# Kernel optimization log

Measured on AMD Instinct MI355X. Metric: run time of the kernel, lower is better.

## Reference

```python
import jax, jax.numpy as jnp
import numpy as np

N_NODES = 100000
N_EDGES = 3200000
F_IN = 256
HID = 64
N_CLS = 16


def setup_inputs() -> dict:
    key = jax.random.key(0)
    ks = jax.random.split(key, 12)
    x = jax.random.normal(ks[0], (N_NODES, F_IN), dtype=jnp.float32)
    edge_index = jax.random.randint(ks[1], (2, N_EDGES), 0, N_NODES, dtype=jnp.int32)
    w_mul = jax.random.normal(ks[2], (N_EDGES, 1), dtype=jnp.float32)
    s1 = 1.0 / np.sqrt(F_IN)
    s2 = 1.0 / np.sqrt(HID)
    # layer 1 params
    lin1_w = jax.random.uniform(ks[3], (HID, F_IN), minval=-s1, maxval=s1, dtype=jnp.float32)
    lin1_b = jax.random.uniform(ks[4], (HID,), minval=-s1, maxval=s1, dtype=jnp.float32)
    mlp1_w0 = jax.random.uniform(ks[5], (HID, 1), minval=-1.0, maxval=1.0, dtype=jnp.float32)
    mlp1_w1 = jax.random.uniform(ks[6], (HID, HID), minval=-s2, maxval=s2, dtype=jnp.float32)
    mlp1_b1 = jax.random.uniform(ks[7], (HID,), minval=-s2, maxval=s2, dtype=jnp.float32)
    # layer 2 params
    lin2_w = jax.random.uniform(ks[8], (N_CLS, HID), minval=-s2, maxval=s2, dtype=jnp.float32)
    lin2_b = jax.random.uniform(ks[9], (N_CLS,), minval=-s2, maxval=s2, dtype=jnp.float32)
    mlp2_w0 = jax.random.uniform(ks[10], (HID, 1), minval=-1.0, maxval=1.0, dtype=jnp.float32)
    mlp2_w1 = jax.random.uniform(ks[11], (N_CLS, HID), minval=-s2, maxval=s2, dtype=jnp.float32)
    mlp2_b1 = jnp.zeros((N_CLS,), dtype=jnp.float32)
    return dict(x=x, edge_index=edge_index, w_mul=w_mul,
                lin1_w=lin1_w, lin1_b=lin1_b, mlp1_w0=mlp1_w0, mlp1_w1=mlp1_w1, mlp1_b1=mlp1_b1,
                lin2_w=lin2_w, lin2_b=lin2_b, mlp2_w0=mlp2_w0, mlp2_w1=mlp2_w1, mlp2_b1=mlp2_b1)


def curv_layer(x, src, dst, w_mul, lin_w, lin_b, m_w0, m_w1, m_b1, n_nodes):
    # dense projection: [N, out]
    h = x @ lin_w.T + lin_b
    # per-edge weight MLP: Linear(1,HID,no bias) -> LeakyReLU(0.2) -> Linear(HID,out,bias)
    ew = jax.nn.leaky_relu(w_mul @ m_w0.T, negative_slope=0.2) @ m_w1.T + m_b1  # [E, out]
    # segment softmax keyed by source node (PyG softmax(out_weight, edge_index[0]))
    emax = jax.ops.segment_max(ew, src, num_segments=n_nodes)  # [N, out]
    e = jnp.exp(ew - emax[src])
    esum = jax.ops.segment_sum(e, src, num_segments=n_nodes)
    alpha = e / (esum[src] + 1e-16)  # [E, out]
    # message = alpha * x_j (x_j = h[src]); scatter-add at destination
    msg = alpha * h[src]
    return jax.ops.segment_sum(msg, dst, num_segments=n_nodes)  # [N, out]


def reference(x, edge_index, w_mul,
              lin1_w, lin1_b, mlp1_w0, mlp1_w1, mlp1_b1,
              lin2_w, lin2_b, mlp2_w0, mlp2_w1, mlp2_b1):
    src, dst = edge_index[0], edge_index[1]
    n = x.shape[0]
    # eval mode: dropout(p=0.8) is identity
    h = curv_layer(x, src, dst, w_mul, lin1_w, lin1_b, mlp1_w0, mlp1_w1, mlp1_b1, n)
    h = jax.nn.elu(h)
    h = curv_layer(h, src, dst, w_mul, lin2_w, lin2_b, mlp2_w0, mlp2_w1, mlp2_b1, n)
    return jax.nn.log_softmax(h, axis=1)
```

## Files before the change

### kernel.cpp

```cpp
#include <hip/hip_runtime.h>
#include <math.h>

#define FIN 256
#define HID 64
#define NCLS 16
#define BSH 8
#define BWD (1 << BSH)
#define NBKMAX 512
#define CAP 9216
#define CHUNK_S 8192
#define CHUNK_D 4096

typedef __attribute__((ext_vector_type(8))) short bf16x8;
typedef __attribute__((ext_vector_type(4))) float f32x4;

__global__ __launch_bounds__(512) void init_kernel(int* gcur_s, int* gcur_d) {
    int tid = threadIdx.x;
    gcur_s[tid] = tid * CAP;
    gcur_d[tid] = tid * CAP;
}

__global__ __launch_bounds__(512) void stage_kernel(const int* __restrict__ ei,
                                                    const float* __restrict__ w,
                                                    int* gcur_s, int* gcur_d,
                                                    unsigned int* st_s, uint2* st_d,
                                                    int E, int nchunk_s) {
    __shared__ int lh[NBKMAX];
    __shared__ int lofs[NBKMAX];
    __shared__ int lcur[NBKMAX];
    __shared__ int gbase[NBKMAX];
    __shared__ int wsum[8];
    __shared__ uint2 buf2[CHUNK_D];
    unsigned int* buf1 = (unsigned int*)buf2;
    int tid = threadIdx.x;
    int wv = tid >> 6, lane = tid & 63;
    int side = (blockIdx.x >= nchunk_s) ? 1 : 0;
    lh[tid] = 0;
    __syncthreads();
    if (!side) {
        int base = blockIdx.x * CHUNK_S;
        #pragma unroll
        for (int j = 0; j < CHUNK_S / 512; j++) {
            int e = base + tid + j * 512;
            if (e < E) atomicAdd(&lh[((unsigned)ei[e]) >> BSH], 1);
        }
    } else {
        int base = (blockIdx.x - nchunk_s) * CHUNK_D;
        #pragma unroll
        for (int j = 0; j < CHUNK_D / 512; j++) {
            int e = base + tid + j * 512;
            if (e < E) atomicAdd(&lh[((unsigned)ei[E + e]) >> BSH], 1);
        }
    }
    __syncthreads();
    int v = lh[tid];
    int inc = v;
    #pragma unroll
    for (int off = 1; off < 64; off <<= 1) {
        int p = __shfl_up(inc, off);
        if (lane >= off) inc += p;
    }
    if (lane == 63) wsum[wv] = inc;
    __syncthreads();
    int pre = 0;
    #pragma unroll
    for (int j = 0; j < 8; j++) pre += (j < wv) ? wsum[j] : 0;
    int ex = pre + inc - v;
    lofs[tid] = ex;
    lcur[tid] = ex;
    __syncthreads();
    if (!side) {
        int base = blockIdx.x * CHUNK_S;
        #pragma unroll
        for (int j = 0; j < CHUNK_S / 512; j++) {
            int e = base + tid + j * 512;
            if (e < E) {
                int s = ei[e];
                unsigned int rec = (__float_as_uint(w[e]) & 0xFFFFFF00u) | (unsigned int)(s & 0xFF);
                int p = atomicAdd(&lcur[((unsigned)s) >> BSH], 1);
                buf1[p] = rec;
            }
        }
    } else {
        int base = (blockIdx.x - nchunk_s) * CHUNK_D;
        #pragma unroll
        for (int j = 0; j < CHUNK_D / 512; j++) {
            int e = base + tid + j * 512;
            if (e < E) {
                int d = ei[E + e];
                int s = ei[e];
                unsigned int rec = (__float_as_uint(w[e]) & 0xFFFFFF00u) | (unsigned int)(d & 0xFF);
                int p = atomicAdd(&lcur[((unsigned)d) >> BSH], 1);
                buf2[p] = make_uint2((unsigned int)s, rec);
            }
        }
    }
    __syncthreads();
    {
        int c = lh[tid];
        if (c) gbase[tid] = atomicAdd(side ? &gcur_d[tid] : &gcur_s[tid], c);
    }
    __syncthreads();
    int sub = lane >> 4, ln = lane & 15;
    if (!side) {
        for (int b0 = wv * 64; b0 < wv * 64 + 64; b0 += 4) {
            int b = b0 + sub;
            int c = lh[b];
            int ls = lofs[b], gs = gbase[b];
            for (int i = ln; i < c; i += 16) st_s[gs + i] = buf1[ls + i];
        }
    } else {
        for (int b0 = wv * 64; b0 < wv * 64 + 64; b0 += 4) {
            int b = b0 + sub;
            int c = lh[b];
            int ls = lofs[b], gs = gbase[b];
            for (int i = ln; i < c; i += 16) st_d[gs + i] = buf2[ls + i];
        }
    }
}

__global__ __launch_bounds__(512) void bucket_scan_kernel(const int* gcur_s, const int* gcur_d,
                                                          int* bbase_s, int* bbase_d,
                                                          int* offs_s, int* offs_d,
                                                          int N, int nbk, int E) {
    int side = blockIdx.x;
    const int* gc = side ? gcur_d : gcur_s;
    int* bb = side ? bbase_d : bbase_s;
    __shared__ int tmp[512];
    int tid = threadIdx.x;
    int v = (tid < nbk) ? (gc[tid] - tid * CAP) : 0;
    tmp[tid] = v;
    __syncthreads();
    for (int off = 1; off < 512; off <<= 1) {
        int add = (tid >= off) ? tmp[tid - off] : 0;
        __syncthreads();
        tmp[tid] += add;
        __syncthreads();
    }
    if (tid < nbk) bb[tid] = tmp[tid] - v;
    if (tid == 0) {
        bb[nbk] = E;
        (side ? offs_d : offs_s)[N] = E;
    }
}

__global__ __launch_bounds__(256) void bucket_build_s_kernel(const int* __restrict__ bbase,
                                                             const unsigned int* __restrict__ st,
                                                             int* offs, int* mid, float* t_s, int N) {
    int b = blockIdx.x;
    int r0 = bbase[b];
    int cnt = bbase[b + 1] - r0;
    if (cnt > CAP) cnt = CAP;
    size_t sb = (size_t)b * CAP;
    int n0 = b << BSH;
    int nn = min(BWD, N - n0);
    __shared__ int lh[2 * BWD];
    __shared__ int lscan[BWD];
    __shared__ int lcur[2 * BWD];
    __shared__ float buf[CAP];
    int tid = threadIdx.x;
    lh[tid] = 0;
    lh[tid + BWD] = 0;
    __syncthreads();
    for (int i = tid; i < cnt; i += 256) {
        unsigned int rec = st[sb + i];
        atomicAdd(&lh[((rec & 0xFFu) << 1) | (rec >> 31)], 1);
    }
    __syncthreads();
    int c0 = lh[2 * tid], c1 = lh[2 * tid + 1];
    int v = c0 + c1;
    lscan[tid] = v;
    __syncthreads();
    for (int off = 1; off < 256; off <<= 1) {
        int add = (tid >= off) ? lscan[tid - off] : 0;
        __syncthreads();
        lscan[tid] += add;
        __syncthreads();
    }
    int ex = lscan[tid] - v;
    if (tid < nn) {
        offs[n0 + tid] = r0 + ex;
        mid[n0 + tid] = r0 + ex + c0;
    }
    lcur[2 * tid] = ex;
    lcur[2 * tid + 1] = ex + c0;
    __syncthreads();
    for (int i = tid; i < cnt; i += 256) {
        unsigned int rec = st[sb + i];
        int p = atomicAdd(&lcur[((rec & 0xFFu) << 1) | (rec >> 31)], 1);
        buf[p] = __uint_as_float(rec & 0xFFFFFF00u);
    }
    __syncthreads();
    for (int i = tid; i < cnt; i += 256) t_s[r0 + i] = buf[i];
}

__global__ __launch_bounds__(256) void bucket_build_d_kernel(const int* __restrict__ bbase,
                                                             const uint2* __restrict__ st,
                                                             int* offs, int2* ed, int N) {
    int b = blockIdx.x;
    int r0 = bbase[b];
    int cnt = bbase[b + 1] - r0;
    if (cnt > CAP) cnt = CAP;
    size_t sb = (size_t)b * CAP;
    int n0 = b << BSH;
    int nn = min(BWD, N - n0);
    __shared__ int lh[BWD];
    __shared__ int lofs[BWD];
    __shared__ int2 buf[CAP];
    int tid = threadIdx.x;
    lh[tid] = 0;
    __syncthreads();
    for (int i = tid; i < cnt; i += 256) atomicAdd(&lh[st[sb + i].y & 0xFFu], 1);
    __syncthreads();
    int v = lh[tid];
    lofs[tid] = v;
    __syncthreads();
    for (int off = 1; off < 256; off <<= 1) {
        int add = (tid >= off) ? lofs[tid - off] : 0;
        __syncthreads();
        lofs[tid] += add;
        __syncthreads();
    }
    int ex = lofs[tid] - v;
    if (tid < nn) offs[n0 + tid] = r0 + ex;
    lofs[tid] = ex;
    __syncthreads();
    for (int i = tid; i < cnt; i += 256) {
        uint2 rec = st[sb + i];
        int p = atomicAdd(&lofs[rec.y & 0xFFu], 1);
        buf[p] = make_int2((int)rec.x, (int)(rec.y & 0xFFFFFF00u));
    }
    __syncthreads();
    for (int i = tid; i < cnt; i += 256) ed[r0 + i] = buf[i];
}

#define LOG2E 1.44269504088896340736f
__global__ void prep_kernel(const float* __restrict__ w0a, const float* __restrict__ w1a,
                            const float* __restrict__ w0b, const float* __restrict__ w1b,
                            float* Ap1, float* An1, float* Ap2, float* An2) {
    int tid = threadIdx.x;
    if (tid < 64) {
        float ap = 0.f, an = 0.f;
        for (int j = 0; j < 64; j++) {
            float w0 = w0a[j];
            float w1 = w1a[tid * 64 + j];
            ap += w0 * ((w0 >= 0.f) ? 1.f : 0.2f) * w1;
            an += w0 * ((w0 <= 0.f) ? 1.f : 0.2f) * w1;
        }
        Ap1[tid] = ap * LOG2E; An1[tid] = an * LOG2E;
    } else if (tid < 80) {
        int k = tid - 64;
        float ap = 0.f, an = 0.f;
        for (int j = 0; j < 64; j++) {
            float w0 = w0b[j];
            float w1 = w1b[k * 64 + j];
            ap += w0 * ((w0 >= 0.f) ? 1.f : 0.2f) * w1;
            an += w0 * ((w0 <= 0.f) ? 1.f : 0.2f) * w1;
        }
        Ap2[k] = ap * LOG2E; An2[k] = an * LOG2E;
    }
}

__device__ __forceinline__ float seg_expsum(const float* __restrict__ t, int i0, int i1, float a) {
    float sum = 0.f;
    int i = i0;
    for (; i + 3 < i1; i += 4) {
        float t0 = t[i], t1 = t[i + 1], t2 = t[i + 2], t3 = t[i + 3];
        sum += __builtin_amdgcn_exp2f(t0 * a);
        sum += __builtin_amdgcn_exp2f(t1 * a);
        sum += __builtin_amdgcn_exp2f(t2 * a);
        sum += __builtin_amdgcn_exp2f(t3 * a);
    }
    for (; i < i1; i++) sum += __builtin_amdgcn_exp2f(t[i] * a);
    return sum;
}

__global__ __launch_bounds__(256) void esum1_kernel(const int* __restrict__ offs,
                                                    const int* __restrict__ mid,
                                                    const float* __restrict__ t_s,
                                                    const float* __restrict__ Ap,
                                                    const float* __restrict__ An,
                                                    float* __restrict__ inv, int N) {
    int node = blockIdx.x * 4 + (threadIdx.x >> 6);
    int k = threadIdx.x & 63;
    if (node >= N) return;
    int s0 = offs[node], m = mid[node], s1 = offs[node + 1];
    float sum = seg_expsum(t_s, s0, m, Ap[k]) + seg_expsum(t_s, m, s1, An[k]);
    inv[(size_t)node * 64 + k] = (s1 > s0) ? 1.f / (sum + 1e-16f) : 0.f;
}

__global__ __launch_bounds__(256) void esum2_kernel(const int* __restrict__ offs,
                                                    const int* __restrict__ mid,
                                                    const float* __restrict__ t_s,
                                                    const float* __restrict__ Ap,
                                                    const float* __restrict__ An,
                                                    float* __restrict__ inv, int N) {
    int node = blockIdx.x * 16 + (threadIdx.x >> 4);
    int k = threadIdx.x & 15;
    if (node >= N) return;
    int s0 = offs[node], m = mid[node], s1 = offs[node + 1];
    float sum = seg_expsum(t_s, s0, m, Ap[k]) + seg_expsum(t_s, m, s1, An[k]);
    inv[(size_t)node * 16 + k] = (s1 > s0) ? 1.f / (sum + 1e-16f) : 0.f;
}

__device__ __forceinline__ unsigned int bf16rn(float f) {
    unsigned int u = __float_as_uint(f);
    return (u + 0x7fffu + ((u >> 16) & 1u)) >> 16;
}

__device__ __forceinline__ void cvt8_split(const float4 a, const float4 b, bf16x8& h, bf16x8& l) {
    float f[8] = {a.x, a.y, a.z, a.w, b.x, b.y, b.z, b.w};
    #pragma unroll
    for (int j = 0; j < 8; j++) {
        unsigned int uh = bf16rn(f[j]);
        float hf = __uint_as_float(uh << 16);
        float r = f[j] - hf;
        unsigned int ul = bf16rn(r);
        h[j] = (short)uh;
        l[j] = (short)ul;
    }
}

#define KCH 64
__global__ __launch_bounds__(256, 4) void gemm1_kernel(const float* __restrict__ x,
                                                       const float* __restrict__ W,
                                                       const float* __restrict__ b,
                                                       const float* __restrict__ inv,
                                                       uint2* __restrict__ g1, int N) {
    __shared__ unsigned short xh[64 * KCH];
    __shared__ unsigned short xl[64 * KCH];
    __shared__ unsigned short wh[64 * KCH];
    __shared__ unsigned short wl[64 * KCH];
    int tid = threadIdx.x;
    int block_row = blockIdx.x * 64;
    float4 pf[4][2];
    auto load_chunk = [&](int kbase) {
        #pragma unroll
        for (int i = 0; i < 4; i++) {
            int t = tid + i * 256;
            if (t < 512) {
                int r = t >> 3, g = t & 7;
                int gr = block_row + r;
                if (gr < N) {
                    const float* p = &x[(size_t)gr * FIN + kbase + g * 8];
                    pf[i][0] = *(const float4*)p;
                    pf[i][1] = *(const float4*)(p + 4);
                } else {
                    pf[i][0] = make_float4(0.f, 0.f, 0.f, 0.f);
                    pf[i][1] = make_float4(0.f, 0.f, 0.f, 0.f);
                }
            } else {
                int r = (t - 512) >> 3, g = t & 7;
                const float* p = &W[r * FIN + kbase + g * 8];
                pf[i][0] = *(const float4*)p;
                pf[i][1] = *(const float4*)(p + 4);
            }
        }
    };
    auto write_chunk = [&]() {
        #pragma unroll
        for (int i = 0; i < 4; i++) {
            int t = tid + i * 256;
            int r = (t & 511) >> 3, g = t & 7;
            int gs = g ^ (r & 7);
            bf16x8 h, l;
            cvt8_split(pf[i][0], pf[i][1], h, l);
            if (t < 512) {
                *(bf16x8*)&xh[r * KCH + gs * 8] = h;
                *(bf16x8*)&xl[r * KCH + gs * 8] = l;
            } else {
                *(bf16x8*)&wh[r * KCH + gs * 8] = h;
                *(bf16x8*)&wl[r * KCH + gs * 8] = l;
            }
        }
    };

    int wv = tid >> 6, l = tid & 63;
    int lrow = l & 15, kg = l >> 4;
    f32x4 acc[4];
    #pragma unroll
    for (int c = 0; c < 4; c++) acc[c] = (f32x4){0.f, 0.f, 0.f, 0.f};

    const unsigned short* xrow_h = &xh[(wv * 16 + lrow) * KCH];
    const unsigned short* xrow_l = &xl[(wv * 16 + lrow) * KCH];

    load_chunk(0);
    for (int kc = 0; kc < FIN / KCH; kc++) {
        write_chunk();
        __syncthreads();
        if (kc + 1 < FIN / KCH) load_chunk((kc + 1) * KCH);
        #pragma unroll
        for (int s = 0; s < 2; s++) {
            int gB = ((s * 4 + kg) ^ (lrow & 7)) * 8;
            bf16x8 bh = *(const bf16x8*)&xrow_h[gB];
            bf16x8 bl = *(const bf16x8*)&xrow_l[gB];
            #pragma unroll
            for (int c = 0; c < 4; c++) {
                int wro = (c * 16 + lrow) * KCH + gB;
                bf16x8 ah = *(const bf16x8*)&wh[wro];
                bf16x8 al = *(const bf16x8*)&wl[wro];
                acc[c] = __builtin_amdgcn_mfma_f32_16x16x32_bf16(ah, bh, acc[c], 0, 0, 0);
                acc[c] = __builtin_amdgcn_mfma_f32_16x16x32_bf16(ah, bl, acc[c], 0, 0, 0);
                acc[c] = __builtin_amdgcn_mfma_f32_16x16x32_bf16(al, bh, acc[c], 0, 0, 0);
            }
        }
        __syncthreads();
    }
    int node = block_row + wv * 16 + lrow;
    if (node < N) {
        #pragma unroll
        for (int c = 0; c < 4; c++) {
            int colb = c * 16 + kg * 4;
            float4 bv = *(const float4*)&b[colb];
            float4 iv = *(const float4*)&inv[(size_t)node * 64 + colb];
            float o0 = (acc[c].x + bv.x) * iv.x;
            float o1 = (acc[c].y + bv.y) * iv.y;
            float o2 = (acc[c].z + bv.z) * iv.z;
            float o3 = (acc[c].w + bv.w) * iv.w;
            uint2 p;
            p.x = bf16rn(o0) | (bf16rn(o1) << 16);
            p.y = bf16rn(o2) | (bf16rn(o3) << 16);
            g1[(size_t)node * 16 + (colb >> 2)] = p;
        }
    }
}

#define GP 68
__global__ __launch_bounds__(256) void gemm2_kernel(const float* __restrict__ x2,
                                                    const float* __restrict__ W2,
                                                    const float* __restrict__ b2,
                                                    const float* __restrict__ inv,
                                                    float* __restrict__ g2, int N) {
    __shared__ float ws[16][GP];
    __shared__ float xs[16][GP];
    __shared__ float bs[16];
    int tid = threadIdx.x;
    {
        int c = tid >> 4, j4 = tid & 15;
        float4 v = ((const float4*)W2)[tid];
        ws[c][j4 * 4 + 0] = v.x; ws[c][j4 * 4 + 1] = v.y;
        ws[c][j4 * 4 + 2] = v.z; ws[c][j4 * 4 + 3] = v.w;
    }
    if (tid < 16) bs[tid] = b2[tid];
    int node0 = blockIdx.x * 16;
    {
        int r = tid >> 4, c4 = tid & 15;
        int gn = node0 + r;
        float4 v = (gn < N) ? *(const float4*)&x2[(size_t)gn * 64 + c4 * 4]
                            : make_float4(0.f, 0.f, 0.f, 0.f);
        xs[r][c4 * 4 + 0] = v.x; xs[r][c4 * 4 + 1] = v.y;
        xs[r][c4 * 4 + 2] = v.z; xs[r][c4 * 4 + 3] = v.w;
    }
    __syncthreads();
    int node_l = tid >> 4, col = tid & 15;
    int gn = node0 + node_l;
    if (gn >= N) return;
    float acc = bs[col];
    #pragma unroll
    for (int j4 = 0; j4 < 16; j4++) {
        float4 xv = *(const float4*)&xs[node_l][j4 * 4];
        float4 wv = *(const float4*)&ws[col][j4 * 4];
        acc += xv.x * wv.x + xv.y * wv.y + xv.z * wv.z + xv.w * wv.w;
    }
    g2[(size_t)gn * NCLS + col] = acc * inv[(size_t)gn * NCLS + col];
}

__global__ __launch_bounds__(256) void agg1_kernel(const int* __restrict__ offs,
                                                   const int2* __restrict__ ed,
                                                   const float* __restrict__ Ap,
                                                   const float* __restrict__ An,
                                                   const uint4* __restrict__ g,
                                                   float* __restrict__ x2, int N) {
    int node = blockIdx.x * 32 + (threadIdx.x >> 3);
    int l = threadIdx.x & 7;
    if (node >= N) return;
    int d0 = offs[node], d1 = offs[node + 1];
    float4 ap0 = ((const float4*)Ap)[l * 2], ap1 = ((const float4*)Ap)[l * 2 + 1];
    float4 an0 = ((const float4*)An)[l * 2], an1 = ((const float4*)An)[l * 2 + 1];
    float4 acc0 = make_float4(0.f, 0.f, 0.f, 0.f);
    float4 acc1 = make_float4(0.f, 0.f, 0.f, 0.f);
    int i = d0;
    int end4 = d0 + ((d1 - d0) & ~3);
    for (; i < end4; i += 4) {
        int2 e[4];
        #pragma unroll
        for (int j = 0; j < 4; j++) e[j] = ed[i + j];
        uint4 gv[4];
        #pragma unroll
        for (int j = 0; j < 4; j++)
            gv[j] = g[((size_t)e[j].x << 3) + l];
        #pragma unroll
        for (int j = 0; j < 4; j++) {
            float t = __int_as_float(e[j].y);
            float4 a0 = (t >= 0.f) ? ap0 : an0;
            float4 a1 = (t >= 0.f) ? ap1 : an1;
            acc0.x += __builtin_amdgcn_exp2f(t * a0.x) * __uint_as_float(gv[j].x << 16);
            acc0.y += __builtin_amdgcn_exp2f(t * a0.y) * __uint_as_float(gv[j].x & 0xffff0000u);
            acc0.z += __builtin_amdgcn_exp2f(t * a0.z) * __uint_as_float(gv[j].y << 16);
            acc0.w += __builtin_amdgcn_exp2f(t * a0.w) * __uint_as_float(gv[j].y & 0xffff0000u);
            acc1.x += __builtin_amdgcn_exp2f(t * a1.x) * __uint_as_float(gv[j].z << 16);
            acc1.y += __builtin_amdgcn_exp2f(t * a1.y) * __uint_as_float(gv[j].z & 0xffff0000u);
            acc1.z += __builtin_amdgcn_exp2f(t * a1.z) * __uint_as_float(gv[j].w << 16);
            acc1.w += __builtin_amdgcn_exp2f(t * a1.w) * __uint_as_float(gv[j].w & 0xffff0000u);
        }
    }
    for (; i < d1; i++) {
        int2 e = ed[i];
        float t = __int_as_float(e.y);
        float4 a0 = (t >= 0.f) ? ap0 : an0;
        float4 a1 = (t >= 0.f) ? ap1 : an1;
        uint4 gv = g[((size_t)e.x << 3) + l];
        acc0.x += __builtin_amdgcn_exp2f(t * a0.x) * __uint_as_float(gv.x << 16);
        acc0.y += __builtin_amdgcn_exp2f(t * a0.y) * __uint_as_float(gv.x & 0xffff0000u);
        acc0.z += __builtin_amdgcn_exp2f(t * a0.z) * __uint_as_float(gv.y << 16);
        acc0.w += __builtin_amdgcn_exp2f(t * a0.w) * __uint_as_float(gv.y & 0xffff0000u);
        acc1.x += __builtin_amdgcn_exp2f(t * a1.x) * __uint_as_float(gv.z << 16);
        acc1.y += __builtin_amdgcn_exp2f(t * a1.y) * __uint_as_float(gv.z & 0xffff0000u);
        acc1.z += __builtin_amdgcn_exp2f(t * a1.z) * __uint_as_float(gv.w << 16);
        acc1.w += __builtin_amdgcn_exp2f(t * a1.w) * __uint_as_float(gv.w & 0xffff0000u);
    }
    float4 o0, o1;
    o0.x = (acc0.x > 0.f) ? acc0.x : (__expf(acc0.x) - 1.f);
    o0.y = (acc0.y > 0.f) ? acc0.y : (__expf(acc0.y) - 1.f);
    o0.z = (acc0.z > 0.f) ? acc0.z : (__expf(acc0.z) - 1.f);
    o0.w = (acc0.w > 0.f) ? acc0.w : (__expf(acc0.w) - 1.f);
    o1.x = (acc1.x > 0.f) ? acc1.x : (__expf(acc1.x) - 1.f);
    o1.y = (acc1.y > 0.f) ? acc1.y : (__expf(acc1.y) - 1.f);
    o1.z = (acc1.z > 0.f) ? acc1.z : (__expf(acc1.z) - 1.f);
    o1.w = (acc1.w > 0.f) ? acc1.w : (__expf(acc1.w) - 1.f);
    float* dst = x2 + ((size_t)node << 6) + l * 8;
    *(float4*)(dst) = o0;
    *(float4*)(dst + 4) = o1;
}

__global__ __launch_bounds__(256) void agg2_kernel(const int* __restrict__ offs,
                                                   const int2* __restrict__ ed,
                                                   const float* __restrict__ Ap,
                                                   const float* __restrict__ An,
                                                   const float* __restrict__ g,
                                                   float* __restrict__ out, int N) {
    int node = blockIdx.x * 64 + (threadIdx.x >> 2);
    int l = threadIdx.x & 3;
    if (node >= N) return;
    int d0 = offs[node], d1 = offs[node + 1];
    float4 ap = ((const float4*)Ap)[l];
    float4 an = ((const float4*)An)[l];
    float4 acc = make_float4(0.f, 0.f, 0.f, 0.f);
    int i = d0;
    int end8 = d0 + ((d1 - d0) & ~7);
    for (; i < end8; i += 8) {
        int2 e[8];
        #pragma unroll
        for (int j = 0; j < 8; j++) e[j] = ed[i + j];
        float4 gv[8];
        #pragma unroll
        for (int j = 0; j < 8; j++)
            gv[j] = *(const float4*)(g + ((size_t)e[j].x << 4) + l * 4);
        #pragma unroll
        for (int j = 0; j < 8; j++) {
            float t = __int_as_float(e[j].y);
            float4 a = (t >= 0.f) ? ap : an;
            acc.x += __builtin_amdgcn_exp2f(t * a.x) * gv[j].x;
            acc.y += __builtin_amdgcn_exp2f(t * a.y) * gv[j].y;
            acc.z += __builtin_amdgcn_exp2f(t * a.z) * gv[j].z;
            acc.w += __builtin_amdgcn_exp2f(t * a.w) * gv[j].w;
        }
    }
    for (; i < d1; i++) {
        int2 e = ed[i];
        float t = __int_as_float(e.y);
        float4 a = (t >= 0.f) ? ap : an;
        float4 gv = *(const float4*)(g + ((size_t)e.x << 4) + l * 4);
        acc.x += __builtin_amdgcn_exp2f(t * a.x) * gv.x;
        acc.y += __builtin_amdgcn_exp2f(t * a.y) * gv.y;
        acc.z += __builtin_amdgcn_exp2f(t * a.z) * gv.z;
        acc.w += __builtin_amdgcn_exp2f(t * a.w) * gv.w;
    }
    float m = fmaxf(fmaxf(acc.x, acc.y), fmaxf(acc.z, acc.w));
    m = fmaxf(m, __shfl_xor(m, 1, 4));
    m = fmaxf(m, __shfl_xor(m, 2, 4));
    float s = __expf(acc.x - m) + __expf(acc.y - m) + __expf(acc.z - m) + __expf(acc.w - m);
    s += __shfl_xor(s, 1, 4);
    s += __shfl_xor(s, 2, 4);
    float lse = m + __logf(s);
    float4 o = make_float4(acc.x - lse, acc.y - lse, acc.z - lse, acc.w - lse);
    *(float4*)(out + ((size_t)node << 4) + l * 4) = o;
}

extern "C" void kernel_launch(void* const* d_in, const int* in_sizes, int n_in,
                              void* d_out, int out_size, void* d_ws, size_t ws_size,
                              hipStream_t stream) {
    const float* x      = (const float*)d_in[0];
    const int*   ei     = (const int*)d_in[1];
    const float* wmul   = (const float*)d_in[2];
    const float* lin1_w = (const float*)d_in[3];
    const float* lin1_b = (const float*)d_in[4];
    const float* m1w0   = (const float*)d_in[5];
    const float* m1w1   = (const float*)d_in[6];
    const float* lin2_w = (const float*)d_in[8];
    const float* lin2_b = (const float*)d_in[9];
    const float* m2w0   = (const float*)d_in[10];
    const float* m2w1   = (const float*)d_in[11];

    int N = in_sizes[0] / FIN;
    int E = in_sizes[1] / 2;
    int nbk = (N + BWD - 1) >> BSH;
    int nchunk_s = (E + CHUNK_S - 1) / CHUNK_S;
    int nchunk_d = (E + CHUNK_D - 1) / CHUNK_D;

    char* ws = (char*)d_ws;
    auto alloc = [&](size_t bytes) {
        char* p = ws;
        ws += (bytes + 255) & ~(size_t)255;
        return p;
    };
    int*   gcur_s  = (int*)alloc(NBKMAX * 4);
    int*   gcur_d  = (int*)alloc(NBKMAX * 4);
    int*   bbase_s = (int*)alloc((NBKMAX + 1) * 4);
    int*   bbase_d = (int*)alloc((NBKMAX + 1) * 4);
    float* Ap1     = (float*)alloc(64 * 4);
    float* An1     = (float*)alloc(64 * 4);
    float* Ap2     = (float*)alloc(16 * 4);
    float* An2     = (float*)alloc(16 * 4);
    int*   offs_s  = (int*)alloc((size_t)(N + 1) * 4);
    int*   offs_d  = (int*)alloc((size_t)(N + 1) * 4);
    int*   mid_s   = (int*)alloc((size_t)N * 4);
    float* t_s     = (float*)alloc((size_t)E * 4);
    int2*  ed      = (int2*)alloc((size_t)E * 8);
    char*  reg = ws;
    unsigned int* st_s = (unsigned int*)(reg);
    uint2*        st_d = (uint2*)(reg + (((size_t)nbk * CAP * 4 + 255) & ~(size_t)255));
    float* inv1 = (float*)(reg);
    float* x2   = (float*)(reg);
    char*  regB = reg + (((size_t)N * 64 * 4 + 255) & ~(size_t)255);
    uint2* g1   = (uint2*)(regB);
    float* inv2 = (float*)(regB + ((size_t)N * 16 * 8));
    float* g2   = (float*)(regB + ((size_t)N * 16 * 8) + ((size_t)N * 16 * 4));

    init_kernel<<<1, 512, 0, stream>>>(gcur_s, gcur_d);
    prep_kernel<<<1, 128, 0, stream>>>(m1w0, m1w1, m2w0, m2w1, Ap1, An1, Ap2, An2);
    stage_kernel<<<nchunk_s + nchunk_d, 512, 0, stream>>>(ei, wmul, gcur_s, gcur_d,
                                                          st_s, st_d, E, nchunk_s);
    bucket_scan_kernel<<<2, 512, 0, stream>>>(gcur_s, gcur_d, bbase_s, bbase_d,
                                              offs_s, offs_d, N, nbk, E);
    bucket_build_s_kernel<<<nbk, 256, 0, stream>>>(bbase_s, st_s, offs_s, mid_s, t_s, N);
    bucket_build_d_kernel<<<nbk, 256, 0, stream>>>(bbase_d, st_d, offs_d, ed, N);
    esum1_kernel<<<(N + 3) / 4, 256, 0, stream>>>(offs_s, mid_s, t_s, Ap1, An1, inv1, N);
    gemm1_kernel<<<(N + 63) / 64, 256, 0, stream>>>(x, lin1_w, lin1_b, inv1, g1, N);
    agg1_kernel<<<(N + 31) / 32, 256, 0, stream>>>(offs_d, ed, Ap1, An1, (const uint4*)g1, x2, N);
    esum2_kernel<<<(N + 15) / 16, 256, 0, stream>>>(offs_s, mid_s, t_s, Ap2, An2, inv2, N);
    gemm2_kernel<<<(N + 15) / 16, 256, 0, stream>>>(x2, lin2_w, lin2_b, inv2, g2, N);
    agg2_kernel<<<(N + 63) / 64, 256, 0, stream>>>(offs_d, ed, Ap2, An2, g2, (float*)d_out, N);
}
```

Baseline: 487.9 us.

## Merge bucket builds and esum passes; fuse agg1 with layer-2 GEMM

Combines the source and destination bucket-build kernels into one 512-thread launch that uses a wave-shuffle scan in place of the shared-memory Hillis-Steele scan. It also merges both esum passes into one launch and fuses agg1 with gemm2, so the layer-1 output x2 stays in shared memory and never makes a round trip through global memory. This cuts launch count, global traffic for x2, and barrier-heavy scans. The trade-offs are more shared memory per block and a larger combined bucket-build buffer (int2), which may lower occupancy.

```diff
diff --git a/kernel.cpp b/kernel.cpp
--- a/kernel.cpp
+++ b/kernel.cpp
@@ -144,94 +144,86 @@
     }
 }
 
-__global__ __launch_bounds__(256) void bucket_build_s_kernel(const int* __restrict__ bbase,
-                                                             const unsigned int* __restrict__ st,
-                                                             int* offs, int* mid, float* t_s, int N) {
-    int b = blockIdx.x;
+__global__ __launch_bounds__(512) void bucket_build_kernel(const int* __restrict__ bbase_s,
+                                                           const int* __restrict__ bbase_d,
+                                                           const unsigned int* __restrict__ st_s,
+                                                           const uint2* __restrict__ st_d,
+                                                           int* offs_s, int* mid_s, int* offs_d,
+                                                           float* t_s, int2* ed, int N, int nbk) {
+    __shared__ int lh[2 * BWD];
+    __shared__ int lcur[2 * BWD];
+    __shared__ int wsum[4];
+    __shared__ int2 buf[CAP];
+    int tid = threadIdx.x;
+    int lane = tid & 63, wv = tid >> 6;
+    int sside = (blockIdx.x < nbk);
+    int b = sside ? blockIdx.x : (blockIdx.x - nbk);
+    const int* bbase = sside ? bbase_s : bbase_d;
     int r0 = bbase[b];
     int cnt = bbase[b + 1] - r0;
     if (cnt > CAP) cnt = CAP;
     size_t sb = (size_t)b * CAP;
     int n0 = b << BSH;
     int nn = min(BWD, N - n0);
-    __shared__ int lh[2 * BWD];
-    __shared__ int lscan[BWD];
-    __shared__ int lcur[2 * BWD];
-    __shared__ float buf[CAP];
-    int tid = threadIdx.x;
     lh[tid] = 0;
-    lh[tid + BWD] = 0;
-    __syncthreads();
-    for (int i = tid; i < cnt; i += 256) {
-        unsigned int rec = st[sb + i];
-        atomicAdd(&lh[((rec & 0xFFu) << 1) | (rec >> 31)], 1);
-    }
-    __syncthreads();
-    int c0 = lh[2 * tid], c1 = lh[2 * tid + 1];
-    int v = c0 + c1;
-    lscan[tid] = v;
-    __syncthreads();
-    for (int off = 1; off < 256; off <<= 1) {
-        int add = (tid >= off) ? lscan[tid - off] : 0;
+    __syncthreads();
+    if (sside) {
+        for (int i = tid; i < cnt; i += 512) {
+            unsigned int rec = st_s[sb + i];
+            atomicAdd(&lh[((rec & 0xFFu) << 1) | (rec >> 31)], 1);
+        }
+    } else {
+        for (int i = tid; i < cnt; i += 512) {
+            atomicAdd(&lh[st_d[sb + i].y & 0xFFu], 1);
+        }
+    }
+    __syncthreads();
+    int c0 = 0, v = 0, inc = 0;
+    if (tid < 256) {
+        if (sside) { c0 = lh[2 * tid]; v = c0 + lh[2 * tid + 1]; }
+        else { v = lh[tid]; }
+        inc = v;
+        #pragma unroll
+        for (int off = 1; off < 64; off <<= 1) {
+            int p = __shfl_up(inc, off);
+            if (lane >= off) inc += p;
+        }
+        if (lane == 63) wsum[wv] = inc;
+    }
+    __syncthreads();
+    if (tid < 256) {
+        int pre = 0;
+        #pragma unroll
+        for (int j = 0; j < 4; j++) pre += (j < wv) ? wsum[j] : 0;
+        int ex = pre + inc - v;
+        if (sside) {
+            if (tid < nn) { offs_s[n0 + tid] = r0 + ex; mid_s[n0 + tid] = r0 + ex + c0; }
+            lcur[2 * tid] = ex;
+            lcur[2 * tid + 1] = ex + c0;
+        } else {
+            if (tid < nn) offs_d[n0 + tid] = r0 + ex;
+            lcur[tid] = ex;
+        }
+    }
+    __syncthreads();
+    if (sside) {
+        float* buff = (float*)buf;
+        for (int i = tid; i < cnt; i += 512) {
+            unsigned int rec = st_s[sb + i];
+            int p = atomicAdd(&lcur[((rec & 0xFFu) << 1) | (rec >> 31)], 1);
+            buff[p] = __uint_as_float(rec & 0xFFFFFF00u);
+        }
         __syncthreads();
-        lscan[tid] += add;
+        for (int i = tid; i < cnt; i += 512) t_s[r0 + i] = buff[i];
+    } else {
+        for (int i = tid; i < cnt; i += 512) {
+            uint2 rec = st_d[sb + i];
+            int p = atomicAdd(&lcur[rec.y & 0xFFu], 1);
+            buf[p] = make_int2((int)rec.x, (int)(rec.y & 0xFFFFFF00u));
+        }
         __syncthreads();
-    }
-    int ex = lscan[tid] - v;
-    if (tid < nn) {
-        offs[n0 + tid] = r0 + ex;
-        mid[n0 + tid] = r0 + ex + c0;
-    }
-    lcur[2 * tid] = ex;
-    lcur[2 * tid + 1] = ex + c0;
-    __syncthreads();
-    for (int i = tid; i < cnt; i += 256) {
-        unsigned int rec = st[sb + i];
-        int p = atomicAdd(&lcur[((rec & 0xFFu) << 1) | (rec >> 31)], 1);
-        buf[p] = __uint_as_float(rec & 0xFFFFFF00u);
-    }
-    __syncthreads();
-    for (int i = tid; i < cnt; i += 256) t_s[r0 + i] = buf[i];
-}
-
-__global__ __launch_bounds__(256) void bucket_build_d_kernel(const int* __restrict__ bbase,
-                                                             const uint2* __restrict__ st,
-                                                             int* offs, int2* ed, int N) {
-    int b = blockIdx.x;
-    int r0 = bbase[b];
-    int cnt = bbase[b + 1] - r0;
-    if (cnt > CAP) cnt = CAP;
-    size_t sb = (size_t)b * CAP;
-    int n0 = b << BSH;
-    int nn = min(BWD, N - n0);
-    __shared__ int lh[BWD];
-    __shared__ int lofs[BWD];
-    __shared__ int2 buf[CAP];
-    int tid = threadIdx.x;
-    lh[tid] = 0;
-    __syncthreads();
-    for (int i = tid; i < cnt; i += 256) atomicAdd(&lh[st[sb + i].y & 0xFFu], 1);
-    __syncthreads();
-    int v = lh[tid];
-    lofs[tid] = v;
-    __syncthreads();
-    for (int off = 1; off < 256; off <<= 1) {
-        int add = (tid >= off) ? lofs[tid - off] : 0;
-        __syncthreads();
-        lofs[tid] += add;
-        __syncthreads();
-    }
-    int ex = lofs[tid] - v;
-    if (tid < nn) offs[n0 + tid] = r0 + ex;
-    lofs[tid] = ex;
-    __syncthreads();
-    for (int i = tid; i < cnt; i += 256) {
-        uint2 rec = st[sb + i];
-        int p = atomicAdd(&lofs[rec.y & 0xFFu], 1);
-        buf[p] = make_int2((int)rec.x, (int)(rec.y & 0xFFFFFF00u));
-    }
-    __syncthreads();
-    for (int i = tid; i < cnt; i += 256) ed[r0 + i] = buf[i];
+        for (int i = tid; i < cnt; i += 512) ed[r0 + i] = buf[i];
+    }
 }
 
 #define LOG2E 1.44269504088896340736f
@@ -275,32 +267,30 @@
     return sum;
 }
 
-__global__ __launch_bounds__(256) void esum1_kernel(const int* __restrict__ offs,
-                                                    const int* __restrict__ mid,
-                                                    const float* __restrict__ t_s,
-                                                    const float* __restrict__ Ap,
-                                                    const float* __restrict__ An,
-                                                    float* __restrict__ inv, int N) {
-    int node = blockIdx.x * 4 + (threadIdx.x >> 6);
-    int k = threadIdx.x & 63;
-    if (node >= N) return;
-    int s0 = offs[node], m = mid[node], s1 = offs[node + 1];
-    float sum = seg_expsum(t_s, s0, m, Ap[k]) + seg_expsum(t_s, m, s1, An[k]);
-    inv[(size_t)node * 64 + k] = (s1 > s0) ? 1.f / (sum + 1e-16f) : 0.f;
-}
-
-__global__ __launch_bounds__(256) void esum2_kernel(const int* __restrict__ offs,
-                                                    const int* __restrict__ mid,
-                                                    const float* __restrict__ t_s,
-                                                    const float* __restrict__ Ap,
-                                                    const float* __restrict__ An,
-                                                    float* __restrict__ inv, int N) {
-    int node = blockIdx.x * 16 + (threadIdx.x >> 4);
-    int k = threadIdx.x & 15;
-    if (node >= N) return;
-    int s0 = offs[node], m = mid[node], s1 = offs[node + 1];
-    float sum = seg_expsum(t_s, s0, m, Ap[k]) + seg_expsum(t_s, m, s1, An[k]);
-    inv[(size_t)node * 16 + k] = (s1 > s0) ? 1.f / (sum + 1e-16f) : 0.f;
+__global__ __launch_bounds__(256) void esum_kernel(const int* __restrict__ offs,
+                                                   const int* __restrict__ mid,
+                                                   const float* __restrict__ t_s,
+                                                   const float* __restrict__ Ap1,
+                                                   const float* __restrict__ An1,
+                                                   const float* __restrict__ Ap2,
+                                                   const float* __restrict__ An2,
+                                                   float* __restrict__ inv1,
+                                                   float* __restrict__ inv2, int N, int nblk1) {
+    if ((int)blockIdx.x < nblk1) {
+        int node = blockIdx.x * 4 + (threadIdx.x >> 6);
+        int k = threadIdx.x & 63;
+        if (node >= N) return;
+        int s0 = offs[node], m = mid[node], s1 = offs[node + 1];
+        float sum = seg_expsum(t_s, s0, m, Ap1[k]) + seg_expsum(t_s, m, s1, An1[k]);
+        inv1[(size_t)node * 64 + k] = (s1 > s0) ? 1.f / (sum + 1e-16f) : 0.f;
+    } else {
+        int node = (blockIdx.x - nblk1) * 16 + (threadIdx.x >> 4);
+        int k = threadIdx.x & 15;
+        if (node >= N) return;
+        int s0 = offs[node], m = mid[node], s1 = offs[node + 1];
+        float sum = seg_expsum(t_s, s0, m, Ap2[k]) + seg_expsum(t_s, m, s1, An2[k]);
+        inv2[(size_t)node * 16 + k] = (s1 > s0) ? 1.f / (sum + 1e-16f) : 0.f;
+    }
 }
 
 __device__ __forceinline__ unsigned int bf16rn(float f) {
@@ -426,13 +416,17 @@
 }
 
 #define GP 68
-__global__ __launch_bounds__(256) void gemm2_kernel(const float* __restrict__ x2,
-                                                    const float* __restrict__ W2,
-                                                    const float* __restrict__ b2,
-                                                    const float* __restrict__ inv,
-                                                    float* __restrict__ g2, int N) {
+__global__ __launch_bounds__(256) void agg1g2_kernel(const int* __restrict__ offs,
+                                                     const int2* __restrict__ ed,
+                                                     const float* __restrict__ Ap,
+                                                     const float* __restrict__ An,
+                                                     const uint4* __restrict__ g,
+                                                     const float* __restrict__ W2,
+                                                     const float* __restrict__ b2,
+                                                     const float* __restrict__ inv2,
+                                                     float* __restrict__ g2, int N) {
+    __shared__ float xs[32][GP];
     __shared__ float ws[16][GP];
-    __shared__ float xs[16][GP];
     __shared__ float bs[16];
     int tid = threadIdx.x;
     {
@@ -442,82 +436,57 @@
         ws[c][j4 * 4 + 2] = v.z; ws[c][j4 * 4 + 3] = v.w;
     }
     if (tid < 16) bs[tid] = b2[tid];
-    int node0 = blockIdx.x * 16;
-    {
-        int r = tid >> 4, c4 = tid & 15;
-        int gn = node0 + r;
-        float4 v = (gn < N) ? *(const float4*)&x2[(size_t)gn * 64 + c4 * 4]
-                            : make_float4(0.f, 0.f, 0.f, 0.f);
-        xs[r][c4 * 4 + 0] = v.x; xs[r][c4 * 4 + 1] = v.y;
-        xs[r][c4 * 4 + 2] = v.z; xs[r][c4 * 4 + 3] = v.w;
-    }
-    __syncthreads();
-    int node_l = tid >> 4, col = tid & 15;
-    int gn = node0 + node_l;
-    if (gn >= N) return;
-    float acc = bs[col];
-    #pragma unroll
-    for (int j4 = 0; j4 < 16; j4++) {
-        float4 xv = *(const float4*)&xs[node_l][j4 * 4];
-        float4 wv = *(const float4*)&ws[col][j4 * 4];
-        acc += xv.x * wv.x + xv.y * wv.y + xv.z * wv.z + xv.w * wv.w;
-    }
-    g2[(size_t)gn * NCLS + col] = acc * inv[(size_t)gn * NCLS + col];
-}
-
-__global__ __launch_bounds__(256) void agg1_kernel(const int* __restrict__ offs,
-                                                   const int2* __restrict__ ed,
-                                                   const float* __restrict__ Ap,
-                                                   const float* __restrict__ An,
-                                                   const uint4* __restrict__ g,
-                                                   float* __restrict__ x2, int N) {
-    int node = blockIdx.x * 32 + (threadIdx.x >> 3);
-    int l = threadIdx.x & 7;
-    if (node >= N) return;
-    int d0 = offs[node], d1 = offs[node + 1];
-    float4 ap0 = ((const float4*)Ap)[l * 2], ap1 = ((const float4*)Ap)[l * 2 + 1];
-    float4 an0 = ((const float4*)An)[l * 2], an1 = ((const float4*)An)[l * 2 + 1];
+
+    int node0 = blockIdx.x * 32;
+    int nl8 = tid >> 3;
+    int node = node0 + nl8;
+    int l = tid & 7;
     float4 acc0 = make_float4(0.f, 0.f, 0.f, 0.f);
     float4 acc1 = make_float4(0.f, 0.f, 0.f, 0.f);
-    int i = d0;
-    int end4 = d0 + ((d1 - d0) & ~3);
-    for (; i < end4; i += 4) {
-        int2 e[4];
-        #pragma unroll
-        for (int j = 0; j < 4; j++) e[j] = ed[i + j];
-        uint4 gv[4];
-        #pragma unroll
-        for (int j = 0; j < 4; j++)
-            gv[j] = g[((size_t)e[j].x << 3) + l];
-        #pragma unroll
-        for (int j = 0; j < 4; j++) {
-            float t = __int_as_float(e[j].y);
+    if (node < N) {
+        int d0 = offs[node], d1 = offs[node + 1];
+        float4 ap0 = ((const float4*)Ap)[l * 2], ap1 = ((const float4*)Ap)[l * 2 + 1];
+        float4 an0 = ((const float4*)An)[l * 2], an1 = ((const float4*)An)[l * 2 + 1];
+        int i = d0;
+        int end4 = d0 + ((d1 - d0) & ~3);
+        for (; i < end4; i += 4) {
+            int2 e[4];
+            #pragma unroll
+            for (int j = 0; j < 4; j++) e[j] = ed[i + j];
+            uint4 gv[4];
+            #pragma unroll
+            for (int j = 0; j < 4; j++)
+                gv[j] = g[((size_t)e[j].x << 3) + l];
+            #pragma unroll
+            for (int j = 0; j < 4; j++) {
+                float t = __int_as_float(e[j].y);
+                float4 a0 = (t >= 0.f) ? ap0 : an0;
+                float4 a1 = (t >= 0.f) ? ap1 : an1;
+                acc0.x += __builtin_amdgcn_exp2f(t * a0.x) * __uint_as_float(gv[j].x << 16);
+                acc0.y += __builtin_amdgcn_exp2f(t * a0.y) * __uint_as_float(gv[j].x & 0xffff0000u);
+                acc0.z += __builtin_amdgcn_exp2f(t * a0.z) * __uint_as_float(gv[j].y << 16);
+                acc0.w += __builtin_amdgcn_exp2f(t * a0.w) * __uint_as_float(gv[j].y & 0xffff0000u);
+                acc1.x += __builtin_amdgcn_exp2f(t * a1.x) * __uint_as_float(gv[j].z << 16);
+                acc1.y += __builtin_amdgcn_exp2f(t * a1.y) * __uint_as_float(gv[j].z & 0xffff0000u);
+                acc1.z += __builtin_amdgcn_exp2f(t * a1.z) * __uint_as_float(gv[j].w << 16);
+                acc1.w += __builtin_amdgcn_exp2f(t * a1.w) * __uint_as_float(gv[j].w & 0xffff0000u);
+            }
+        }
+        for (; i < d1; i++) {
+            int2 e = ed[i];
+            float t = __int_as_float(e.y);
             float4 a0 = (t >= 0.f) ? ap0 : an0;
             float4 a1 = (t >= 0.f) ? ap1 : an1;
-            acc0.x += __builtin_amdgcn_exp2f(t * a0.x) * __uint_as_float(gv[j].x << 16);
-            acc0.y += __builtin_amdgcn_exp2f(t * a0.y) * __uint_as_float(gv[j].x & 0xffff0000u);
-            acc0.z += __builtin_amdgcn_exp2f(t * a0.z) * __uint_as_float(gv[j].y << 16);
-            acc0.w += __builtin_amdgcn_exp2f(t * a0.w) * __uint_as_float(gv[j].y & 0xffff0000u);
-            acc1.x += __builtin_amdgcn_exp2f(t * a1.x) * __uint_as_float(gv[j].z << 16);
-            acc1.y += __builtin_amdgcn_exp2f(t * a1.y) * __uint_as_float(gv[j].z & 0xffff0000u);
-            acc1.z += __builtin_amdgcn_exp2f(t * a1.z) * __uint_as_float(gv[j].w << 16);
-            acc1.w += __builtin_amdgcn_exp2f(t * a1.w) * __uint_as_float(gv[j].w & 0xffff0000u);
-        }
-    }
-    for (; i < d1; i++) {
-        int2 e = ed[i];
-        float t = __int_as_float(e.y);
-        float4 a0 = (t >= 0.f) ? ap0 : an0;
-        float4 a1 = (t >= 0.f) ? ap1 : an1;
-        uint4 gv = g[((size_t)e.x << 3) + l];
-        acc0.x += __builtin_amdgcn_exp2f(t * a0.x) * __uint_as_float(gv.x << 16);
-        acc0.y += __builtin_amdgcn_exp2f(t * a0.y) * __uint_as_float(gv.x & 0xffff0000u);
-        acc0.z += __builtin_amdgcn_exp2f(t * a0.z) * __uint_as_float(gv.y << 16);
-        acc0.w += __builtin_amdgcn_exp2f(t * a0.w) * __uint_as_float(gv.y & 0xffff0000u);
-        acc1.x += __builtin_amdgcn_exp2f(t * a1.x) * __uint_as_float(gv.z << 16);
-        acc1.y += __builtin_amdgcn_exp2f(t * a1.y) * __uint_as_float(gv.z & 0xffff0000u);
-        acc1.z += __builtin_amdgcn_exp2f(t * a1.z) * __uint_as_float(gv.w << 16);
-        acc1.w += __builtin_amdgcn_exp2f(t * a1.w) * __uint_as_float(gv.w & 0xffff0000u);
+            uint4 gv = g[((size_t)e.x << 3) + l];
+            acc0.x += __builtin_amdgcn_exp2f(t * a0.x) * __uint_as_float(gv.x << 16);
+            acc0.y += __builtin_amdgcn_exp2f(t * a0.y) * __uint_as_float(gv.x & 0xffff0000u);
+            acc0.z += __builtin_amdgcn_exp2f(t * a0.z) * __uint_as_float(gv.y << 16);
+            acc0.w += __builtin_amdgcn_exp2f(t * a0.w) * __uint_as_float(gv.y & 0xffff0000u);
+            acc1.x += __builtin_amdgcn_exp2f(t * a1.x) * __uint_as_float(gv.z << 16);
+            acc1.y += __builtin_amdgcn_exp2f(t * a1.y) * __uint_as_float(gv.z & 0xffff0000u);
+            acc1.z += __builtin_amdgcn_exp2f(t * a1.z) * __uint_as_float(gv.w << 16);
+            acc1.w += __builtin_amdgcn_exp2f(t * a1.w) * __uint_as_float(gv.w & 0xffff0000u);
+        }
     }
     float4 o0, o1;
     o0.x = (acc0.x > 0.f) ? acc0.x : (__expf(acc0.x) - 1.f);
@@ -528,9 +497,25 @@
     o1.y = (acc1.y > 0.f) ? acc1.y : (__expf(acc1.y) - 1.f);
     o1.z = (acc1.z > 0.f) ? acc1.z : (__expf(acc1.z) - 1.f);
     o1.w = (acc1.w > 0.f) ? acc1.w : (__expf(acc1.w) - 1.f);
-    float* dst = x2 + ((size_t)node << 6) + l * 8;
-    *(float4*)(dst) = o0;
-    *(float4*)(dst + 4) = o1;
+    *(float4*)&xs[nl8][l * 8] = o0;
+    *(float4*)&xs[nl8][l * 8 + 4] = o1;
+    __syncthreads();
+    int col = tid & 15;
+    #pragma unroll
+    for (int h = 0; h < 2; h++) {
+        int nl = (tid >> 4) + h * 16;
+        int gn = node0 + nl;
+        if (gn < N) {
+            float acc = bs[col];
+            #pragma unroll
+            for (int j4 = 0; j4 < 16; j4++) {
+                float4 xv = *(const float4*)&xs[nl][j4 * 4];
+                float4 wv = *(const float4*)&ws[col][j4 * 4];
+                acc += xv.x * wv.x + xv.y * wv.y + xv.z * wv.z + xv.w * wv.w;
+            }
+            g2[(size_t)gn * NCLS + col] = acc * inv2[(size_t)gn * NCLS + col];
+        }
+    }
 }
 
 __global__ __launch_bounds__(256) void agg2_kernel(const int* __restrict__ offs,
@@ -631,11 +616,13 @@
     unsigned int* st_s = (unsigned int*)(reg);
     uint2*        st_d = (uint2*)(reg + (((size_t)nbk * CAP * 4 + 255) & ~(size_t)255));
     float* inv1 = (float*)(reg);
-    float* x2   = (float*)(reg);
     char*  regB = reg + (((size_t)N * 64 * 4 + 255) & ~(size_t)255);
     uint2* g1   = (uint2*)(regB);
     float* inv2 = (float*)(regB + ((size_t)N * 16 * 8));
     float* g2   = (float*)(regB + ((size_t)N * 16 * 8) + ((size_t)N * 16 * 4));
+
+    int nblk1 = (N + 3) / 4;
+    int nblk2 = (N + 15) / 16;
 
     init_kernel<<<1, 512, 0, stream>>>(gcur_s, gcur_d);
     prep_kernel<<<1, 128, 0, stream>>>(m1w0, m1w1, m2w0, m2w1, Ap1, An1, Ap2, An2);
@@ -643,12 +630,12 @@
                                                           st_s, st_d, E, nchunk_s);
     bucket_scan_kernel<<<2, 512, 0, stream>>>(gcur_s, gcur_d, bbase_s, bbase_d,
                                               offs_s, offs_d, N, nbk, E);
-    bucket_build_s_kernel<<<nbk, 256, 0, stream>>>(bbase_s, st_s, offs_s, mid_s, t_s, N);
-    bucket_build_d_kernel<<<nbk, 256, 0, stream>>>(bbase_d, st_d, offs_d, ed, N);
-    esum1_kernel<<<(N + 3) / 4, 256, 0, stream>>>(offs_s, mid_s, t_s, Ap1, An1, inv1, N);
+    bucket_build_kernel<<<2 * nbk, 512, 0, stream>>>(bbase_s, bbase_d, st_s, st_d,
+                                                     offs_s, mid_s, offs_d, t_s, ed, N, nbk);
+    esum_kernel<<<nblk1 + nblk2, 256, 0, stream>>>(offs_s, mid_s, t_s, Ap1, An1, Ap2, An2,
+                                                   inv1, inv2, N, nblk1);
     gemm1_kernel<<<(N + 63) / 64, 256, 0, stream>>>(x, lin1_w, lin1_b, inv1, g1, N);
-    agg1_kernel<<<(N + 31) / 32, 256, 0, stream>>>(offs_d, ed, Ap1, An1, (const uint4*)g1, x2, N);
-    esum2_kernel<<<(N + 15) / 16, 256, 0, stream>>>(offs_s, mid_s, t_s, Ap2, An2, inv2, N);
-    gemm2_kernel<<<(N + 15) / 16, 256, 0, stream>>>(x2, lin2_w, lin2_b, inv2, g2, N);
+    agg1g2_kernel<<<(N + 31) / 32, 256, 0, stream>>>(offs_d, ed, Ap1, An1, (const uint4*)g1,
+                                                     lin2_w, lin2_b, inv2, g2, N);
     agg2_kernel<<<(N + 63) / 64, 256, 0, stream>>>(offs_d, ed, Ap2, An2, g2, (float*)d_out, N);
 }
```

Measured after the change: 461.7 us. -5.4%, faster.
